# Kernel tuning notes

Measured on AMD Instinct MI355X. Metric: run time of the kernel, lower is better.

The kernel has to match this reference:

```python
import jax, jax.numpy as jnp
import numpy as np

B, T, E, D = 32, 8192, 256, 32  # batch, seq, embed_dim, output_dim
H, M = D, 2 * D                 # SSM hidden_dim, mlp_dim


def _ssm_block(x, Win, bin_, log_a, Wout, bout, W1, b1, W2, b2):
    """Diagonal linear SSM scan + residual MLP. x: (B,T,D) -> (B,T,D)."""
    u = x @ Win + bin_                      # (B,T,H)
    a = jax.nn.sigmoid(log_a)               # (H,) per-channel decay in (0,1)
    aa = jnp.broadcast_to(a, u.shape)

    def comb(c1, c2):
        a1, h1 = c1
        a2, h2 = c2
        return a1 * a2, a2 * h1 + h2

    _, h = jax.lax.associative_scan(comb, (aa, u), axis=1)  # h_t = a*h_{t-1} + u_t
    y = h @ Wout + bout                      # (B,T,D)
    return y + jax.nn.gelu(y @ W1 + b1) @ W2 + b2


def setup_inputs() -> dict:
    key = jax.random.key(0)
    ks = jax.random.split(key, 20)
    s_in, s_d, s_m = 1.0 / np.sqrt(E), 1.0 / np.sqrt(D), 1.0 / np.sqrt(M)
    inp = {
        "e_seq": jax.random.normal(ks[0], (B, T, E), dtype=jnp.float32),
        "Wpi": jax.random.normal(ks[1], (E, D), dtype=jnp.float32) * s_in,
        "bpi": jnp.zeros((D,), jnp.float32),
        "Wpo": jax.random.normal(ks[2], (2 * D, D), dtype=jnp.float32) * s_d,
        "bpo": jnp.zeros((D,), jnp.float32),
    }
    for i, pfx in enumerate(["f", "b"]):
        o = 3 + 8 * i
        inp[pfx + "_Win"] = jax.random.normal(ks[o], (D, H), dtype=jnp.float32) * s_d
        inp[pfx + "_bin"] = jnp.zeros((H,), jnp.float32)
        inp[pfx + "_loga"] = jax.random.normal(ks[o + 1], (H,), dtype=jnp.float32)
        inp[pfx + "_Wout"] = jax.random.normal(ks[o + 2], (H, D), dtype=jnp.float32) * s_d
        inp[pfx + "_bout"] = jnp.zeros((D,), jnp.float32)
        inp[pfx + "_W1"] = jax.random.normal(ks[o + 3], (D, M), dtype=jnp.float32) * s_d
        inp[pfx + "_b1"] = jnp.zeros((M,), jnp.float32)
        inp[pfx + "_W2"] = jax.random.normal(ks[o + 4], (M, D), dtype=jnp.float32) * s_m
        inp[pfx + "_b2"] = jnp.zeros((D,), jnp.float32)
    return inp


def reference(e_seq, Wpi, bpi, Wpo, bpo,
              f_Win, f_bin, f_loga, f_Wout, f_bout, f_W1, f_b1, f_W2, f_b2,
              b_Win, b_bin, b_loga, b_Wout, b_bout, b_W1, b_b1, b_W2, b_b2):
    x = e_seq @ Wpi + bpi                                    # (B,T,D)
    fwd = _ssm_block(x, f_Win, f_bin, f_loga, f_Wout, f_bout, f_W1, f_b1, f_W2, f_b2)
    bwd = _ssm_block(x[:, ::-1], b_Win, b_bin, b_loga, b_Wout, b_bout,
                     b_W1, b_b1, b_W2, b_b2)[:, ::-1]
    combined = jnp.concatenate([fwd, bwd], axis=-1)           # (B,T,2D)
    return combined @ Wpo + bpo                               # (B,T,D)
```

## Files before the change

kernel.cpp:

```cpp
#include <hip/hip_runtime.h>


typedef unsigned short u16;
typedef unsigned int   u32;
typedef __bf16 bf16x8 __attribute__((ext_vector_type(8)));
typedef float  f32x4  __attribute__((ext_vector_type(4)));

constexpr int BB = 32, TT = 8192, NCH = 64;
constexpr int BT = BB * TT;
constexpr int LCH = 256;
constexpr int NCHUNK = TT / LCH;

#define MFMA16(av, bv, cc) __builtin_amdgcn_mfma_f32_16x16x32_bf16((av), (bv), (cc), 0, 0, 0)

__device__ __forceinline__ u16 f2bf(float x) {
    union { float f; u32 u; } v; v.f = x;
    u32 r = (v.u + 0x7FFFu + ((v.u >> 16) & 1u)) >> 16;
    return (u16)r;
}
__device__ __forceinline__ float bf2f(u16 x) {
    union { u32 u; float f; } v; v.u = ((u32)x) << 16;
    return v.f;
}
__device__ __forceinline__ float gelu_tanh(float x) {
    float inner = 0.7978845608028654f * fmaf(0.044715f * x, x * x, x);
    float ez = __expf(2.f * inner);
    float t = 1.f - 2.f / (ez + 1.f);
    return 0.5f * x * (1.f + t);
}

__global__ void k0_prep(const float* __restrict__ Wpi, const float* __restrict__ bpi,
                        const float* __restrict__ fWin, const float* __restrict__ fbin,
                        const float* __restrict__ floga,
                        const float* __restrict__ bWin, const float* __restrict__ bbin,
                        const float* __restrict__ bloga,
                        const float* __restrict__ fW1, const float* __restrict__ bW1,
                        const float* __restrict__ fW2, const float* __restrict__ bW2,
                        const float* __restrict__ fb2, const float* __restrict__ bb2,
                        const float* __restrict__ fWout, const float* __restrict__ bWout,
                        const float* __restrict__ Wpo, const float* __restrict__ bpo,
                        u16* __restrict__ WuT, float* __restrict__ bu,
                        float* __restrict__ a_arr, float* __restrict__ l2a,
                        u16* __restrict__ W1Tbf, u16* __restrict__ W2poCatT,
                        u16* __restrict__ WoutTbf, u16* __restrict__ WpoCatT,
                        float* __restrict__ bc)
{
    const int blk = blockIdx.x, tid = threadIdx.x;
    if (blk < 64) {
        const float* Win = (blk < 32) ? fWin : bWin;
        const int nn = blk & 31;
        float s = 0.f;
        #pragma unroll
        for (int d = 0; d < 32; ++d) s = fmaf(Wpi[tid * 32 + d], Win[d * 32 + nn], s);
        WuT[blk * 256 + tid] = f2bf(s);
        if (tid == 0) {
            const float* bin = (blk < 32) ? fbin : bbin;
            float sb = bin[nn];
            for (int d = 0; d < 32; ++d) sb = fmaf(bpi[d], Win[d * 32 + nn], sb);
            bu[blk] = sb;
        }
    } else if (blk == 64) {
        if (tid < 64) {
            const float* lg = (tid < 32) ? floga : bloga;
            float a = 1.f / (1.f + __expf(-lg[tid & 31]));
            a_arr[tid] = a;
            l2a[tid] = log2f(a);
        } else if (tid < 96) {
            int i = tid - 64;
            float s = bpo[i];
            for (int d = 0; d < 32; ++d) s = fmaf(fb2[d], Wpo[d * 32 + i], s);
            for (int d = 0; d < 32; ++d) s = fmaf(bb2[d], Wpo[(32 + d) * 32 + i], s);
            bc[i] = s;
        }
    } else if (blk == 65 || blk == 66) {
        int dir = blk - 65;
        const float* W1 = dir ? bW1 : fW1;
        for (int x = tid; x < 2048; x += 256) {
            int n = x >> 5, k = x & 31;
            W1Tbf[dir * 2048 + n * 32 + k] = f2bf(W1[k * 64 + n]);
        }
    } else if (blk == 67 || blk == 68) {
        int dir = blk - 67;
        const float* W2 = dir ? bW2 : fW2;
        const float* Wp = Wpo + dir * 32 * 32;
        for (int x = tid; x < 2048; x += 256) {
            int j = x >> 5, i = x & 31;
            float s = 0.f;
            for (int d = 0; d < 32; ++d) s = fmaf(W2[j * 32 + d], Wp[d * 32 + i], s);
            W2poCatT[i * 128 + dir * 64 + j] = f2bf(s);
        }
    } else if (blk == 69 || blk == 70) {
        int dir = blk - 69;
        const float* Wout = dir ? bWout : fWout;
        for (int x = tid; x < 1024; x += 256) {
            int n = x >> 5, k = x & 31;
            WoutTbf[dir * 1024 + n * 32 + k] = f2bf(Wout[k * 32 + n]);
        }
    } else {
        for (int x = tid; x < 2048; x += 256) {
            int n = x >> 6, k = x & 63;
            WpoCatT[n * 64 + k] = f2bf(Wpo[k * 32 + n]);
        }
    }
}

__global__ __launch_bounds__(256) void kA_proj_scan(const float* __restrict__ e,
    const u16* __restrict__ WuT, const float* __restrict__ bu,
    const float* __restrict__ a_arr, const float* __restrict__ l2a,
    u16* __restrict__ h, float* __restrict__ Ebuf)
{
    __shared__ __align__(16) u16 As[32][264];
    __shared__ __align__(16) u16 utile[256 * 64];
    __shared__ float eSub[64][4];
    const int tid = threadIdx.x;
    const int blk = blockIdx.x;
    const size_t t0 = (size_t)blk * 256;
    const int lane = tid & 63, wave = tid >> 6;
    const int row16 = lane & 15, quad = lane >> 4;
    const int wr = (wave & 1) * 16;
    const int wc = (wave >> 1) * 32;

    #pragma unroll 1
    for (int s = 0; s < 8; ++s) {
        const float4* eg = reinterpret_cast<const float4*>(e + (t0 + s * 32) * 256);
        #pragma unroll
        for (int it = 0; it < 8; ++it) {
            int i = tid + it * 256;
            int r = i >> 6, kk = (i & 63) << 2;
            float4 v = eg[i];
            uint2 pk;
            pk.x = (u32)f2bf(v.x) | ((u32)f2bf(v.y) << 16);
            pk.y = (u32)f2bf(v.z) | ((u32)f2bf(v.w) << 16);
            *reinterpret_cast<uint2*>(&As[r][kk]) = pk;
        }
        __syncthreads();
        f32x4 acc[2] = {{0.f,0.f,0.f,0.f},{0.f,0.f,0.f,0.f}};
        #pragma unroll
        for (int ks = 0; ks < 8; ++ks) {
            bf16x8 av = *reinterpret_cast<const bf16x8*>(&As[wr + row16][ks * 32 + quad * 8]);
            #pragma unroll
            for (int c2 = 0; c2 < 2; ++c2) {
                bf16x8 bv = *reinterpret_cast<const bf16x8*>(WuT + (wc + c2 * 16 + row16) * 256 + ks * 32 + quad * 8);
                acc[c2] = MFMA16(av, bv, acc[c2]);
            }
        }
        #pragma unroll
        for (int c2 = 0; c2 < 2; ++c2) {
            int col = wc + c2 * 16 + row16;
            float bias = bu[col];
            #pragma unroll
            for (int r = 0; r < 4; ++r) {
                int trow = s * 32 + wr + quad * 4 + r;
                utile[trow * 64 + col] = f2bf(acc[c2][r] + bias);
            }
        }
        __syncthreads();
    }

    const int ch = tid & 63, sid = tid >> 6;
    const float a = a_arr[ch];
    const bool fwd = (ch < 32);
    float hh = 0.f;
    if (fwd) {
        for (int i = 0; i < 64; ++i) { int t = sid * 64 + i;
            hh = fmaf(a, hh, bf2f(utile[t * 64 + ch])); utile[t * 64 + ch] = f2bf(hh); }
    } else {
        for (int i = 63; i >= 0; --i) { int t = sid * 64 + i;
            hh = fmaf(a, hh, bf2f(utile[t * 64 + ch])); utile[t * 64 + ch] = f2bf(hh); }
    }
    eSub[ch][sid] = hh;
    __syncthreads();
    const float A = exp2f(64.f * l2a[ch]);
    float cin = 0.f;
    if (fwd) { for (int j = 0; j < sid; ++j) cin = fmaf(A, cin, eSub[ch][j]); }
    else     { for (int j = 3; j > sid; --j) cin = fmaf(A, cin, eSub[ch][j]); }
    if (fwd && sid == 3)  Ebuf[(size_t)blk * 64 + ch] = fmaf(A, cin, eSub[ch][3]);
    if (!fwd && sid == 0) Ebuf[(size_t)blk * 64 + ch] = fmaf(A, cin, eSub[ch][0]);
    float p = cin;
    if (fwd) {
        for (int i = 0; i < 64; ++i) { int t = sid * 64 + i; p *= a;
            utile[t * 64 + ch] = f2bf(bf2f(utile[t * 64 + ch]) + p); }
    } else {
        for (int i = 63; i >= 0; --i) { int t = sid * 64 + i; p *= a;
            utile[t * 64 + ch] = f2bf(bf2f(utile[t * 64 + ch]) + p); }
    }
    __syncthreads();
    uint4* gw = reinterpret_cast<uint4*>(h + t0 * 64);
    const uint4* s4 = reinterpret_cast<const uint4*>(utile);
    #pragma unroll
    for (int i = 0; i < 8; ++i) gw[tid + 256 * i] = s4[tid + 256 * i];
}

__global__ void k3_carry(const float* __restrict__ Ebuf, float* __restrict__ Cin,
                         const float* __restrict__ l2a)
{
    int tid = blockIdx.x * 256 + threadIdx.x;
    if (tid >= BB * NCH) return;
    int b = tid >> 6, ch = tid & 63;
    float aL = exp2f((float)LCH * l2a[ch]);
    float S = 0.f;
    if (ch < 32) {
        for (int c = 0; c < NCHUNK; ++c) {
            size_t idx = ((size_t)(b * NCHUNK + c)) * 64 + ch;
            Cin[idx] = S; S = fmaf(aL, S, Ebuf[idx]);
        }
    } else {
        for (int c = NCHUNK - 1; c >= 0; --c) {
            size_t idx = ((size_t)(b * NCHUNK + c)) * 64 + ch;
            Cin[idx] = S; S = fmaf(aL, S, Ebuf[idx]);
        }
    }
}

__global__ __launch_bounds__(256) void kB_out(const u16* __restrict__ h,
    const float* __restrict__ Cin, const float* __restrict__ l2a,
    const u16* __restrict__ WoutTbf, const float* __restrict__ fbout, const float* __restrict__ bbout,
    const u16* __restrict__ W1Tbf, const float* __restrict__ fb1, const float* __restrict__ bb1,
    const u16* __restrict__ WpoCatT, const u16* __restrict__ W2poCatT,
    const float* __restrict__ bc, float* __restrict__ out)
{
    __shared__ __align__(16) u16 Yt[256 * 64];
    __shared__ __align__(16) u16 Zw[4][16 * 128];
    const int tid = threadIdx.x;
    const int blk = blockIdx.x;
    const size_t t0 = (size_t)blk * 256;
    const int lane = tid & 63, wave = tid >> 6;
    const int row16 = lane & 15, quad = lane >> 4;
    const float* cinp = Cin + (size_t)blk * 64;

    #pragma unroll 1
    for (int rr = 0; rr < 4; ++rr) {
        const int rt = wave * 4 + rr;
        const int kpos = rt * 16 + row16;
        #pragma unroll
        for (int dir = 0; dir < 2; ++dir) {
            uint4 hv = *reinterpret_cast<const uint4*>(h + (t0 + kpos) * 64 + dir * 32 + quad * 8);
            u32 hw[4] = {hv.x, hv.y, hv.z, hv.w};
            const float off = dir ? (float)(LCH - kpos) : (float)(kpos + 1);
            union { bf16x8 v; u16 s[8]; } af;
            #pragma unroll
            for (int j = 0; j < 8; ++j) {
                int chn = dir * 32 + quad * 8 + j;
                float f = bf2f((u16)((hw[j >> 1] >> ((j & 1) * 16)) & 0xFFFFu));
                f = fmaf(cinp[chn], exp2f(off * l2a[chn]), f);
                af.s[j] = f2bf(f);
            }
            f32x4 yv[2] = {{0.f,0.f,0.f,0.f},{0.f,0.f,0.f,0.f}};
            #pragma unroll
            for (int nt = 0; nt < 2; ++nt) {
                bf16x8 bv = *reinterpret_cast<const bf16x8*>(WoutTbf + dir * 1024 + (nt * 16 + row16) * 32 + quad * 8);
                yv[nt] = MFMA16(af.v, bv, yv[nt]);
            }
            const float* boutp = dir ? bbout : fbout;
            #pragma unroll
            for (int nt = 0; nt < 2; ++nt) {
                float bb = boutp[nt * 16 + row16];
                #pragma unroll
                for (int r = 0; r < 4; ++r) {
                    int row = rt * 16 + quad * 4 + r;
                    int col = dir * 32 + nt * 16 + row16;
                    int cs = (col >> 3) ^ (row & 7);
                    Yt[row * 64 + cs * 8 + (col & 7)] = f2bf(yv[nt][r] + bb);
                }
            }
        }
    }

    #pragma unroll 1
    for (int rr = 0; rr < 4; ++rr) {
        const int rt = wave * 4 + rr;
        const int arow = rt * 16 + row16;
        f32x4 o0 = {0.f,0.f,0.f,0.f}, o1 = {0.f,0.f,0.f,0.f};

        #pragma unroll
        for (int kb = 0; kb < 2; ++kb) {
            int cs = (kb * 4 + quad) ^ (arow & 7);
            bf16x8 av = *reinterpret_cast<const bf16x8*>(&Yt[arow * 64 + cs * 8]);
            bf16x8 bv0 = *reinterpret_cast<const bf16x8*>(WpoCatT + (row16) * 64 + kb * 32 + quad * 8);
            bf16x8 bv1 = *reinterpret_cast<const bf16x8*>(WpoCatT + (16 + row16) * 64 + kb * 32 + quad * 8);
            o0 = MFMA16(av, bv0, o0);
            o1 = MFMA16(av, bv1, o1);
        }
        #pragma unroll
        for (int dir = 0; dir < 2; ++dir) {
            int cs = (dir * 4 + quad) ^ (arow & 7);
            bf16x8 av = *reinterpret_cast<const bf16x8*>(&Yt[arow * 64 + cs * 8]);
            const float* b1p = dir ? bb1 : fb1;
            #pragma unroll
            for (int nt2 = 0; nt2 < 4; ++nt2) {
                f32x4 z = {0.f,0.f,0.f,0.f};
                bf16x8 bv = *reinterpret_cast<const bf16x8*>(W1Tbf + dir * 2048 + (nt2 * 16 + row16) * 32 + quad * 8);
                z = MFMA16(av, bv, z);
                float bb = b1p[nt2 * 16 + row16];
                #pragma unroll
                for (int r = 0; r < 4; ++r) {
                    float zz = gelu_tanh(z[r] + bb);
                    int zrow = quad * 4 + r;
                    int zcol = dir * 64 + nt2 * 16 + row16;
                    int zcs = (zcol >> 3) ^ (zrow & 7);
                    Zw[wave][zrow * 128 + zcs * 8 + (zcol & 7)] = f2bf(zz);
                }
            }
        }
        #pragma unroll
        for (int kb = 0; kb < 4; ++kb) {
            int zcs = (kb * 4 + quad) ^ (row16 & 7);
            bf16x8 av = *reinterpret_cast<const bf16x8*>(&Zw[wave][row16 * 128 + zcs * 8]);
            bf16x8 bv0 = *reinterpret_cast<const bf16x8*>(W2poCatT + (row16) * 128 + kb * 32 + quad * 8);
            bf16x8 bv1 = *reinterpret_cast<const bf16x8*>(W2poCatT + (16 + row16) * 128 + kb * 32 + quad * 8);
            o0 = MFMA16(av, bv0, o0);
            o1 = MFMA16(av, bv1, o1);
        }
        #pragma unroll
        for (int r = 0; r < 4; ++r) {
            size_t row = t0 + rt * 16 + quad * 4 + r;
            out[row * 32 + row16]      = o0[r] + bc[row16];
            out[row * 32 + 16 + row16] = o1[r] + bc[16 + row16];
        }
    }
}

extern "C" void kernel_launch(void* const* d_in, const int* in_sizes, int n_in,
                              void* d_out, int out_size, void* d_ws, size_t ws_size,
                              hipStream_t stream)
{
    (void)in_sizes; (void)n_in; (void)out_size; (void)ws_size;
    const float* e     = (const float*)d_in[0];
    const float* Wpi   = (const float*)d_in[1];
    const float* bpi   = (const float*)d_in[2];
    const float* Wpo   = (const float*)d_in[3];
    const float* bpo   = (const float*)d_in[4];
    const float* fWin  = (const float*)d_in[5];
    const float* fbin  = (const float*)d_in[6];
    const float* floga = (const float*)d_in[7];
    const float* fWout = (const float*)d_in[8];
    const float* fbout = (const float*)d_in[9];
    const float* fW1   = (const float*)d_in[10];
    const float* fb1   = (const float*)d_in[11];
    const float* fW2   = (const float*)d_in[12];
    const float* fb2   = (const float*)d_in[13];
    const float* bWin  = (const float*)d_in[14];
    const float* bbin  = (const float*)d_in[15];
    const float* bloga = (const float*)d_in[16];
    const float* bWout = (const float*)d_in[17];
    const float* bbout = (const float*)d_in[18];
    const float* bW1   = (const float*)d_in[19];
    const float* bb1   = (const float*)d_in[20];
    const float* bW2   = (const float*)d_in[21];
    const float* bb2   = (const float*)d_in[22];
    float* outp = (float*)d_out;

    char* ws = (char*)d_ws;
    size_t off = 0;
    auto walloc = [&](size_t bytes) { void* p = ws + off; off += (bytes + 255) & ~(size_t)255; return p; };
    u16*   hbuf  = (u16*)  walloc((size_t)BT * 64 * 2);
    u16*   WuT   = (u16*)  walloc(64 * 256 * 2);
    float* bu    = (float*)walloc(64 * 4);
    float* a_arr = (float*)walloc(64 * 4);
    float* l2a   = (float*)walloc(64 * 4);
    float* Ebuf  = (float*)walloc((size_t)BB * NCHUNK * 64 * 4);
    float* Cin   = (float*)walloc((size_t)BB * NCHUNK * 64 * 4);
    u16*   W1Tbf    = (u16*)walloc(2 * 64 * 32 * 2);
    u16*   W2poCatT = (u16*)walloc(32 * 128 * 2);
    u16*   WoutTbf  = (u16*)walloc(2 * 32 * 32 * 2);
    u16*   WpoCatT  = (u16*)walloc(32 * 64 * 2);
    float* bc    = (float*)walloc(32 * 4);

    k0_prep<<<72, 256, 0, stream>>>(Wpi, bpi, fWin, fbin, floga, bWin, bbin, bloga,
                                    fW1, bW1, fW2, bW2, fb2, bb2, fWout, bWout, Wpo, bpo,
                                    WuT, bu, a_arr, l2a, W1Tbf, W2poCatT, WoutTbf, WpoCatT, bc);
    kA_proj_scan<<<BB * NCHUNK, 256, 0, stream>>>(e, WuT, bu, a_arr, l2a, hbuf, Ebuf);
    k3_carry<<<8, 256, 0, stream>>>(Ebuf, Cin, l2a);
    kB_out<<<BB * NCHUNK, 256, 0, stream>>>(hbuf, Cin, l2a,
                                            WoutTbf, fbout, bbout,
                                            W1Tbf, fb1, bb1,
                                            WpoCatT, W2poCatT, bc, outp);
}
```

Baseline: 467.6 us.

## Widen projection-scan blocks, register-cache weights, shrink kB_out shared memory

The projection+scan kernel now runs 512 threads per block. Each pass loads 64 rows of e, the WuT B-fragments are held in registers for the whole block, and only the first 256 threads do the scan. The carry kernel preloads all chunk end-states into registers before its serial recurrence. The output kernel gives each wave its own small Y tile, fusing its two loops and cutting LDS so more blocks fit per CU. The goals are more memory-level parallelism and higher occupancy, at the cost of more registers and half the threads idling during the scan.

```diff
diff --git a/kernel.cpp b/kernel.cpp
--- a/kernel.cpp
+++ b/kernel.cpp
@@ -104,12 +104,12 @@
     }
 }
 
-__global__ __launch_bounds__(256) void kA_proj_scan(const float* __restrict__ e,
+__global__ __launch_bounds__(512, 4) void kA_proj_scan(const float* __restrict__ e,
     const u16* __restrict__ WuT, const float* __restrict__ bu,
     const float* __restrict__ a_arr, const float* __restrict__ l2a,
     u16* __restrict__ h, float* __restrict__ Ebuf)
 {
-    __shared__ __align__(16) u16 As[32][264];
+    __shared__ __align__(16) u16 As[64][264];
     __shared__ __align__(16) u16 utile[256 * 64];
     __shared__ float eSub[64][4];
     const int tid = threadIdx.x;
@@ -117,15 +117,22 @@
     const size_t t0 = (size_t)blk * 256;
     const int lane = tid & 63, wave = tid >> 6;
     const int row16 = lane & 15, quad = lane >> 4;
-    const int wr = (wave & 1) * 16;
-    const int wc = (wave >> 1) * 32;
+    const int wr = (wave & 3) * 16;
+    const int wc = (wave >> 2) * 32;
+
+    bf16x8 bvv[8][2];
+    #pragma unroll
+    for (int ks = 0; ks < 8; ++ks)
+        #pragma unroll
+        for (int c2 = 0; c2 < 2; ++c2)
+            bvv[ks][c2] = *reinterpret_cast<const bf16x8*>(WuT + (wc + c2 * 16 + row16) * 256 + ks * 32 + quad * 8);
 
     #pragma unroll 1
-    for (int s = 0; s < 8; ++s) {
-        const float4* eg = reinterpret_cast<const float4*>(e + (t0 + s * 32) * 256);
+    for (int s = 0; s < 4; ++s) {
+        const float4* eg = reinterpret_cast<const float4*>(e + (t0 + s * 64) * 256);
         #pragma unroll
         for (int it = 0; it < 8; ++it) {
-            int i = tid + it * 256;
+            int i = tid + it * 512;
             int r = i >> 6, kk = (i & 63) << 2;
             float4 v = eg[i];
             uint2 pk;
@@ -139,10 +146,8 @@
         for (int ks = 0; ks < 8; ++ks) {
             bf16x8 av = *reinterpret_cast<const bf16x8*>(&As[wr + row16][ks * 32 + quad * 8]);
             #pragma unroll
-            for (int c2 = 0; c2 < 2; ++c2) {
-                bf16x8 bv = *reinterpret_cast<const bf16x8*>(WuT + (wc + c2 * 16 + row16) * 256 + ks * 32 + quad * 8);
-                acc[c2] = MFMA16(av, bv, acc[c2]);
-            }
+            for (int c2 = 0; c2 < 2; ++c2)
+                acc[c2] = MFMA16(av, bvv[ks][c2], acc[c2]);
         }
         #pragma unroll
         for (int c2 = 0; c2 < 2; ++c2) {
@@ -150,45 +155,49 @@
             float bias = bu[col];
             #pragma unroll
             for (int r = 0; r < 4; ++r) {
-                int trow = s * 32 + wr + quad * 4 + r;
+                int trow = s * 64 + wr + quad * 4 + r;
                 utile[trow * 64 + col] = f2bf(acc[c2][r] + bias);
             }
         }
         __syncthreads();
     }
 
-    const int ch = tid & 63, sid = tid >> 6;
+    const int ch = tid & 63, sid = (tid >> 6) & 3;
     const float a = a_arr[ch];
     const bool fwd = (ch < 32);
-    float hh = 0.f;
-    if (fwd) {
-        for (int i = 0; i < 64; ++i) { int t = sid * 64 + i;
-            hh = fmaf(a, hh, bf2f(utile[t * 64 + ch])); utile[t * 64 + ch] = f2bf(hh); }
-    } else {
-        for (int i = 63; i >= 0; --i) { int t = sid * 64 + i;
-            hh = fmaf(a, hh, bf2f(utile[t * 64 + ch])); utile[t * 64 + ch] = f2bf(hh); }
-    }
-    eSub[ch][sid] = hh;
+    if (tid < 256) {
+        float hh = 0.f;
+        if (fwd) {
+            for (int i = 0; i < 64; ++i) { int t = sid * 64 + i;
+                hh = fmaf(a, hh, bf2f(utile[t * 64 + ch])); utile[t * 64 + ch] = f2bf(hh); }
+        } else {
+            for (int i = 63; i >= 0; --i) { int t = sid * 64 + i;
+                hh = fmaf(a, hh, bf2f(utile[t * 64 + ch])); utile[t * 64 + ch] = f2bf(hh); }
+        }
+        eSub[ch][sid] = hh;
+    }
     __syncthreads();
-    const float A = exp2f(64.f * l2a[ch]);
-    float cin = 0.f;
-    if (fwd) { for (int j = 0; j < sid; ++j) cin = fmaf(A, cin, eSub[ch][j]); }
-    else     { for (int j = 3; j > sid; --j) cin = fmaf(A, cin, eSub[ch][j]); }
-    if (fwd && sid == 3)  Ebuf[(size_t)blk * 64 + ch] = fmaf(A, cin, eSub[ch][3]);
-    if (!fwd && sid == 0) Ebuf[(size_t)blk * 64 + ch] = fmaf(A, cin, eSub[ch][0]);
-    float p = cin;
-    if (fwd) {
-        for (int i = 0; i < 64; ++i) { int t = sid * 64 + i; p *= a;
-            utile[t * 64 + ch] = f2bf(bf2f(utile[t * 64 + ch]) + p); }
-    } else {
-        for (int i = 63; i >= 0; --i) { int t = sid * 64 + i; p *= a;
-            utile[t * 64 + ch] = f2bf(bf2f(utile[t * 64 + ch]) + p); }
+    if (tid < 256) {
+        const float A = exp2f(64.f * l2a[ch]);
+        float cin = 0.f;
+        if (fwd) { for (int j = 0; j < sid; ++j) cin = fmaf(A, cin, eSub[ch][j]); }
+        else     { for (int j = 3; j > sid; --j) cin = fmaf(A, cin, eSub[ch][j]); }
+        if (fwd && sid == 3)  Ebuf[(size_t)blk * 64 + ch] = fmaf(A, cin, eSub[ch][3]);
+        if (!fwd && sid == 0) Ebuf[(size_t)blk * 64 + ch] = fmaf(A, cin, eSub[ch][0]);
+        float p = cin;
+        if (fwd) {
+            for (int i = 0; i < 64; ++i) { int t = sid * 64 + i; p *= a;
+                utile[t * 64 + ch] = f2bf(bf2f(utile[t * 64 + ch]) + p); }
+        } else {
+            for (int i = 63; i >= 0; --i) { int t = sid * 64 + i; p *= a;
+                utile[t * 64 + ch] = f2bf(bf2f(utile[t * 64 + ch]) + p); }
+        }
     }
     __syncthreads();
     uint4* gw = reinterpret_cast<uint4*>(h + t0 * 64);
     const uint4* s4 = reinterpret_cast<const uint4*>(utile);
     #pragma unroll
-    for (int i = 0; i < 8; ++i) gw[tid + 256 * i] = s4[tid + 256 * i];
+    for (int i = 0; i < 4; ++i) gw[tid + 512 * i] = s4[tid + 512 * i];
 }
 
 __global__ void k3_carry(const float* __restrict__ Ebuf, float* __restrict__ Cin,
@@ -198,28 +207,32 @@
     if (tid >= BB * NCH) return;
     int b = tid >> 6, ch = tid & 63;
     float aL = exp2f((float)LCH * l2a[ch]);
+    const size_t base = (size_t)b * NCHUNK * 64 + ch;
+    float ev[NCHUNK];
+    #pragma unroll
+    for (int c = 0; c < NCHUNK; ++c) ev[c] = Ebuf[base + (size_t)c * 64];
     float S = 0.f;
     if (ch < 32) {
+        #pragma unroll
         for (int c = 0; c < NCHUNK; ++c) {
-            size_t idx = ((size_t)(b * NCHUNK + c)) * 64 + ch;
-            Cin[idx] = S; S = fmaf(aL, S, Ebuf[idx]);
+            Cin[base + (size_t)c * 64] = S; S = fmaf(aL, S, ev[c]);
         }
     } else {
+        #pragma unroll
         for (int c = NCHUNK - 1; c >= 0; --c) {
-            size_t idx = ((size_t)(b * NCHUNK + c)) * 64 + ch;
-            Cin[idx] = S; S = fmaf(aL, S, Ebuf[idx]);
-        }
-    }
-}
-
-__global__ __launch_bounds__(256) void kB_out(const u16* __restrict__ h,
+            Cin[base + (size_t)c * 64] = S; S = fmaf(aL, S, ev[c]);
+        }
+    }
+}
+
+__global__ __launch_bounds__(256, 4) void kB_out(const u16* __restrict__ h,
     const float* __restrict__ Cin, const float* __restrict__ l2a,
     const u16* __restrict__ WoutTbf, const float* __restrict__ fbout, const float* __restrict__ bbout,
     const u16* __restrict__ W1Tbf, const float* __restrict__ fb1, const float* __restrict__ bb1,
     const u16* __restrict__ WpoCatT, const u16* __restrict__ W2poCatT,
     const float* __restrict__ bc, float* __restrict__ out)
 {
-    __shared__ __align__(16) u16 Yt[256 * 64];
+    __shared__ __align__(16) u16 Yt[4][16 * 64];
     __shared__ __align__(16) u16 Zw[4][16 * 128];
     const int tid = threadIdx.x;
     const int blk = blockIdx.x;
@@ -227,11 +240,14 @@
     const int lane = tid & 63, wave = tid >> 6;
     const int row16 = lane & 15, quad = lane >> 4;
     const float* cinp = Cin + (size_t)blk * 64;
+    u16* myY = Yt[wave];
+    u16* myZ = Zw[wave];
 
     #pragma unroll 1
     for (int rr = 0; rr < 4; ++rr) {
         const int rt = wave * 4 + rr;
         const int kpos = rt * 16 + row16;
+
         #pragma unroll
         for (int dir = 0; dir < 2; ++dir) {
             uint4 hv = *reinterpret_cast<const uint4*>(h + (t0 + kpos) * 64 + dir * 32 + quad * 8);
@@ -257,25 +273,20 @@
                 float bb = boutp[nt * 16 + row16];
                 #pragma unroll
                 for (int r = 0; r < 4; ++r) {
-                    int row = rt * 16 + quad * 4 + r;
+                    int row = quad * 4 + r;
                     int col = dir * 32 + nt * 16 + row16;
                     int cs = (col >> 3) ^ (row & 7);
-                    Yt[row * 64 + cs * 8 + (col & 7)] = f2bf(yv[nt][r] + bb);
+                    myY[row * 64 + cs * 8 + (col & 7)] = f2bf(yv[nt][r] + bb);
                 }
             }
         }
-    }
-
-    #pragma unroll 1
-    for (int rr = 0; rr < 4; ++rr) {
-        const int rt = wave * 4 + rr;
-        const int arow = rt * 16 + row16;
+
         f32x4 o0 = {0.f,0.f,0.f,0.f}, o1 = {0.f,0.f,0.f,0.f};
 
         #pragma unroll
         for (int kb = 0; kb < 2; ++kb) {
-            int cs = (kb * 4 + quad) ^ (arow & 7);
-            bf16x8 av = *reinterpret_cast<const bf16x8*>(&Yt[arow * 64 + cs * 8]);
+            int cs = (kb * 4 + quad) ^ (row16 & 7);
+            bf16x8 av = *reinterpret_cast<const bf16x8*>(&myY[row16 * 64 + cs * 8]);
             bf16x8 bv0 = *reinterpret_cast<const bf16x8*>(WpoCatT + (row16) * 64 + kb * 32 + quad * 8);
             bf16x8 bv1 = *reinterpret_cast<const bf16x8*>(WpoCatT + (16 + row16) * 64 + kb * 32 + quad * 8);
             o0 = MFMA16(av, bv0, o0);
@@ -283,8 +294,8 @@
         }
         #pragma unroll
         for (int dir = 0; dir < 2; ++dir) {
-            int cs = (dir * 4 + quad) ^ (arow & 7);
-            bf16x8 av = *reinterpret_cast<const bf16x8*>(&Yt[arow * 64 + cs * 8]);
+            int cs = (dir * 4 + quad) ^ (row16 & 7);
+            bf16x8 av = *reinterpret_cast<const bf16x8*>(&myY[row16 * 64 + cs * 8]);
             const float* b1p = dir ? bb1 : fb1;
             #pragma unroll
             for (int nt2 = 0; nt2 < 4; ++nt2) {
@@ -298,14 +309,14 @@
                     int zrow = quad * 4 + r;
                     int zcol = dir * 64 + nt2 * 16 + row16;
                     int zcs = (zcol >> 3) ^ (zrow & 7);
-                    Zw[wave][zrow * 128 + zcs * 8 + (zcol & 7)] = f2bf(zz);
+                    myZ[zrow * 128 + zcs * 8 + (zcol & 7)] = f2bf(zz);
                 }
             }
         }
         #pragma unroll
         for (int kb = 0; kb < 4; ++kb) {
             int zcs = (kb * 4 + quad) ^ (row16 & 7);
-            bf16x8 av = *reinterpret_cast<const bf16x8*>(&Zw[wave][row16 * 128 + zcs * 8]);
+            bf16x8 av = *reinterpret_cast<const bf16x8*>(&myZ[row16 * 128 + zcs * 8]);
             bf16x8 bv0 = *reinterpret_cast<const bf16x8*>(W2poCatT + (row16) * 128 + kb * 32 + quad * 8);
             bf16x8 bv1 = *reinterpret_cast<const bf16x8*>(W2poCatT + (16 + row16) * 128 + kb * 32 + quad * 8);
             o0 = MFMA16(av, bv0, o0);
@@ -369,7 +380,7 @@
     k0_prep<<<72, 256, 0, stream>>>(Wpi, bpi, fWin, fbin, floga, bWin, bbin, bloga,
                                     fW1, bW1, fW2, bW2, fb2, bb2, fWout, bWout, Wpo, bpo,
                                     WuT, bu, a_arr, l2a, W1Tbf, W2poCatT, WoutTbf, WpoCatT, bc);
-    kA_proj_scan<<<BB * NCHUNK, 256, 0, stream>>>(e, WuT, bu, a_arr, l2a, hbuf, Ebuf);
+    kA_proj_scan<<<BB * NCHUNK, 512, 0, stream>>>(e, WuT, bu, a_arr, l2a, hbuf, Ebuf);
     k3_carry<<<8, 256, 0, stream>>>(Ebuf, Cin, l2a);
     kB_out<<<BB * NCHUNK, 256, 0, stream>>>(hbuf, Cin, l2a,
                                             WoutTbf, fbout, bbout,
```

Result: slower. 543.1 us (+16.1%).
